# Performance work log

Measured on AMD Instinct MI355X. Metric: run time of the kernel, lower is better.

## Reference

```python
import jax, jax.numpy as jnp
import numpy as np

N = 100000   # num nodes
E = 1000000  # num edges
IN = 64      # in_channels
H = 64       # hidden_dim
RESCUE_SCALE = 0.01


def setup_inputs() -> dict:
    key = jax.random.key(0)
    ks = jax.random.split(key, 8)
    x = jax.random.normal(ks[0], (N, IN), jnp.float32)
    edge_index = jax.random.randint(ks[1], (2, E), 0, N, dtype=jnp.int64)
    edge_weight = jax.random.uniform(ks[2], (E,), jnp.float32)
    glorot = lambda k, sh, fan: jax.random.normal(k, sh, jnp.float32) / np.sqrt(fan).astype(np.float32)
    W1 = glorot(ks[3], (IN, H), IN); b1 = jnp.zeros((H,), jnp.float32)
    W2 = glorot(ks[4], (H, H), H);  b2 = jnp.zeros((H,), jnp.float32)
    Wn = glorot(ks[5], (H, 1), H);  bn = jnp.zeros((1,), jnp.float32)
    Wr = glorot(ks[6], (H, 1), H);  br = jnp.zeros((1,), jnp.float32)
    return {"x": x, "edge_index": edge_index, "edge_weight": edge_weight,
            "W1": W1, "b1": b1, "W2": W2, "b2": b2,
            "Wn": Wn, "bn": bn, "Wr": Wr, "br": br}


def gcn_conv(x, src, dst, ew, W, b):
    # PyG GCNConv: linear first, then symmetric-normalized scatter-add aggregation.
    x = x @ W                                              # [N, H]
    deg = jax.ops.segment_sum(ew, dst, num_segments=N)     # weighted in-degree
    dinv = jnp.where(deg > 0, jax.lax.rsqrt(deg), 0.0)     # deg^{-1/2}, inf -> 0
    norm = dinv[src] * ew * dinv[dst]                      # [E+N]
    out = jax.ops.segment_sum(x[src] * norm[:, None], dst, num_segments=N)
    return out + b


def reference(x, edge_index, edge_weight, W1, b1, W2, b2, Wn, bn, Wr, br):
    # add self-loops with weight 1 (GCNConv default)
    loop = jnp.arange(N, dtype=edge_index.dtype)
    src = jnp.concatenate([edge_index[0], loop])
    dst = jnp.concatenate([edge_index[1], loop])
    ew = jnp.concatenate([edge_weight, jnp.ones((N,), edge_weight.dtype)])

    h = jax.nn.relu(gcn_conv(x, src, dst, ew, W1, b1))
    h = jax.nn.relu(gcn_conv(h, src, dst, ew, W2, b2))

    node_logits = (h @ Wn + bn).squeeze(-1)                # [N]
    node_selector = jax.nn.softmax(node_logits, axis=0)
    rescue_ratios = jax.nn.sigmoid((h @ Wr + br).squeeze(-1)) * RESCUE_SCALE
    return node_selector, rescue_ratios
```

## Files before the change

### kernel.cpp

```cpp
#include <hip/hip_runtime.h>
#include <hip/hip_fp16.h>
#include <math.h>

#define NN 100000
#define NE 1000000
#define CAP 32
#define OVCAP 4096
#define NEB 3907
#define NTILE 6250
#define RB 256

typedef _Float16 half8 __attribute__((ext_vector_type(8)));
typedef float f32x4 __attribute__((ext_vector_type(4)));


__global__ __launch_bounds__(256) void k_bucket(const int* __restrict__ src,
                                                const int* __restrict__ dst,
                                                const float* __restrict__ ew,
                                                int* __restrict__ cnt,
                                                int2* __restrict__ bucket,
                                                int4* __restrict__ ovf,
                                                int* __restrict__ ovf_n) {
  int e = blockIdx.x * 256 + threadIdx.x;
  if (e < NE) {
    int s = src[e];
    int d = dst[e];
    float w = ew[e];
    int pos = atomicAdd(&cnt[d], 1);
    if (pos < CAP) {
      bucket[d * CAP + pos] = make_int2(s, __float_as_int(w));
    } else {
      int t = atomicAdd(ovf_n, 1);
      if (t < OVCAP) ovf[t] = make_int4(s, d, __float_as_int(w), 0);
    }
  }
}


__global__ __launch_bounds__(256) void k_degsum(const int* __restrict__ cnt,
                                                const int2* __restrict__ bucket,
                                                const int4* __restrict__ ovf,
                                                const int* __restrict__ ovf_n,
                                                float* __restrict__ dinv) {
  int i = blockIdx.x * 256 + threadIdx.x;
  if (i >= NN) return;
  int c = cnt[i];
  int cc = c < CAP ? c : CAP;
  float dsum = 1.0f;
  const int2* bk = bucket + (size_t)i * CAP;
  for (int j = 0; j < cc; ++j) dsum += __int_as_float(bk[j].y);
  if (c > CAP) {
    int on = ovf_n[0]; if (on > OVCAP) on = OVCAP;
    for (int t = 0; t < on; ++t) {
      int4 o = ovf[t];
      if (o.y == i) dsum += __int_as_float(o.z);
    }
  }
  dinv[i] = 1.0f / sqrtf(dsum);
}


__device__ __forceinline__ void stage_B_lds(const float* __restrict__ W,
                                            _Float16* __restrict__ ldsB) {
  for (int u = threadIdx.x; u < 512; u += 256) {
    int slane = u & 63, ts = u >> 6;
    int t = ts >> 1, s = ts & 1;
    int qq = slane >> 4, ll = slane & 15;
#pragma unroll
    for (int j = 0; j < 8; ++j)
      ldsB[u * 8 + j] = (_Float16)W[(s * 32 + qq * 8 + j) * 64 + t * 16 + ll];
  }
}

__global__ __launch_bounds__(256) void k_gemm_mfma_f32(const float* __restrict__ X,
                                                       const float* __restrict__ W,
                                                       const float* __restrict__ dinv,
                                                       __half* __restrict__ Y) {
  __shared__ _Float16 ldsB[4096];
  stage_B_lds(W, ldsB);
  __syncthreads();
  int lane = threadIdx.x & 63;
  int l15 = lane & 15, q = lane >> 4;
  half8 bfr[4][2];
#pragma unroll
  for (int t = 0; t < 4; ++t)
#pragma unroll
    for (int s = 0; s < 2; ++s)
      bfr[t][s] = *(half8*)&ldsB[((t * 2 + s) * 64 + lane) * 8];

  int wid = blockIdx.x * 4 + (threadIdx.x >> 6);
  for (int tile = wid; tile < NTILE; tile += 2048) {
    int row = tile * 16 + l15;
    f32x4 acc[4] = {{0.f,0.f,0.f,0.f},{0.f,0.f,0.f,0.f},
                    {0.f,0.f,0.f,0.f},{0.f,0.f,0.f,0.f}};
#pragma unroll
    for (int s = 0; s < 2; ++s) {
      const float* ap = X + (size_t)row * 64 + s * 32 + q * 8;
      float4 a0 = *(const float4*)ap;
      float4 a1 = *(const float4*)(ap + 4);
      half8 af;
      af[0] = (_Float16)a0.x; af[1] = (_Float16)a0.y;
      af[2] = (_Float16)a0.z; af[3] = (_Float16)a0.w;
      af[4] = (_Float16)a1.x; af[5] = (_Float16)a1.y;
      af[6] = (_Float16)a1.z; af[7] = (_Float16)a1.w;
#pragma unroll
      for (int t = 0; t < 4; ++t)
        acc[t] = __builtin_amdgcn_mfma_f32_16x16x32_f16(af, bfr[t][s], acc[t], 0, 0, 0);
    }
#pragma unroll
    for (int r = 0; r < 4; ++r) {
      int rw = tile * 16 + q * 4 + r;
      float dv = dinv[rw];
#pragma unroll
      for (int t = 0; t < 4; ++t)
        Y[(size_t)rw * 64 + t * 16 + l15] = __float2half(acc[t][r] * dv);
    }
  }
}

__global__ __launch_bounds__(256) void k_gemm_mfma_f16(const __half* __restrict__ X,
                                                       const float* __restrict__ W,
                                                       const float* __restrict__ dinv,
                                                       __half* __restrict__ Y) {
  __shared__ _Float16 ldsB[4096];
  stage_B_lds(W, ldsB);
  __syncthreads();
  int lane = threadIdx.x & 63;
  int l15 = lane & 15, q = lane >> 4;
  half8 bfr[4][2];
#pragma unroll
  for (int t = 0; t < 4; ++t)
#pragma unroll
    for (int s = 0; s < 2; ++s)
      bfr[t][s] = *(half8*)&ldsB[((t * 2 + s) * 64 + lane) * 8];

  int wid = blockIdx.x * 4 + (threadIdx.x >> 6);
  for (int tile = wid; tile < NTILE; tile += 2048) {
    int row = tile * 16 + l15;
    f32x4 acc[4] = {{0.f,0.f,0.f,0.f},{0.f,0.f,0.f,0.f},
                    {0.f,0.f,0.f,0.f},{0.f,0.f,0.f,0.f}};
#pragma unroll
    for (int s = 0; s < 2; ++s) {
      half8 af = *(const half8*)((const _Float16*)X + (size_t)row * 64 + s * 32 + q * 8);
#pragma unroll
      for (int t = 0; t < 4; ++t)
        acc[t] = __builtin_amdgcn_mfma_f32_16x16x32_f16(af, bfr[t][s], acc[t], 0, 0, 0);
    }
#pragma unroll
    for (int r = 0; r < 4; ++r) {
      int rw = tile * 16 + q * 4 + r;
      float dv = dinv[rw];
#pragma unroll
      for (int t = 0; t < 4; ++t)
        Y[(size_t)rw * 64 + t * 16 + l15] = __float2half(acc[t][r] * dv);
    }
  }
}


__device__ __forceinline__ float4 h4load(const __half* p) {
  float2 raw = *(const float2*)p;
  __half2 a = *(__half2*)&raw.x;
  __half2 b = *(__half2*)&raw.y;
  float2 fa = __half22float2(a), fb = __half22float2(b);
  return make_float4(fa.x, fa.y, fb.x, fb.y);
}

__device__ __forceinline__ float4 gather_node(const __half* __restrict__ xw,
                                              const int* __restrict__ cnt,
                                              const int2* __restrict__ bucket,
                                              const int4* __restrict__ ovf,
                                              const int* __restrict__ ovf_n,
                                              int node, int l) {
  int c = cnt[node];
  int cc = c < CAP ? c : CAP;
  const int4* bk4 = (const int4*)(bucket + (size_t)node * CAP);
  float4 acc = make_float4(0.f, 0.f, 0.f, 0.f);

  int j = 0;
  for (; j + 4 <= cc; j += 4) {
    int4 pa = bk4[j >> 1];
    int4 pb = bk4[(j >> 1) + 1];
    const float4 x0 = h4load(xw + (size_t)pa.x * 64 + l * 4);
    const float4 x1 = h4load(xw + (size_t)pa.z * 64 + l * 4);
    const float4 x2 = h4load(xw + (size_t)pb.x * 64 + l * 4);
    const float4 x3 = h4load(xw + (size_t)pb.z * 64 + l * 4);
    float v0 = __int_as_float(pa.y);
    float v1 = __int_as_float(pa.w);
    float v2 = __int_as_float(pb.y);
    float v3 = __int_as_float(pb.w);
    acc.x = fmaf(x0.x, v0, acc.x); acc.y = fmaf(x0.y, v0, acc.y);
    acc.z = fmaf(x0.z, v0, acc.z); acc.w = fmaf(x0.w, v0, acc.w);
    acc.x = fmaf(x1.x, v1, acc.x); acc.y = fmaf(x1.y, v1, acc.y);
    acc.z = fmaf(x1.z, v1, acc.z); acc.w = fmaf(x1.w, v1, acc.w);
    acc.x = fmaf(x2.x, v2, acc.x); acc.y = fmaf(x2.y, v2, acc.y);
    acc.z = fmaf(x2.z, v2, acc.z); acc.w = fmaf(x2.w, v2, acc.w);
    acc.x = fmaf(x3.x, v3, acc.x); acc.y = fmaf(x3.y, v3, acc.y);
    acc.z = fmaf(x3.z, v3, acc.z); acc.w = fmaf(x3.w, v3, acc.w);
  }
  const int2* bk = (const int2*)bk4;
  for (; j < cc; ++j) {
    int2 E = bk[j];
    const float4 xa = h4load(xw + (size_t)E.x * 64 + l * 4);
    float v = __int_as_float(E.y);
    acc.x = fmaf(xa.x, v, acc.x); acc.y = fmaf(xa.y, v, acc.y);
    acc.z = fmaf(xa.z, v, acc.z); acc.w = fmaf(xa.w, v, acc.w);
  }
  if (c > CAP) {
    int on = ovf_n[0]; if (on > OVCAP) on = OVCAP;
    for (int t = 0; t < on; ++t) {
      int4 o = ovf[t];
      if (o.y == node) {
        const float4 xa = h4load(xw + (size_t)o.x * 64 + l * 4);
        float v = __int_as_float(o.z);
        acc.x = fmaf(xa.x, v, acc.x); acc.y = fmaf(xa.y, v, acc.y);
        acc.z = fmaf(xa.z, v, acc.z); acc.w = fmaf(xa.w, v, acc.w);
      }
    }
  }
  const float4 xs = h4load(xw + (size_t)node * 64 + l * 4);
  acc.x += xs.x; acc.y += xs.y; acc.z += xs.z; acc.w += xs.w;
  return acc;
}


__global__ __launch_bounds__(256) void k_gather_l1(const __half* __restrict__ xw,
                                                   const float* __restrict__ dinv,
                                                   const int* __restrict__ cnt,
                                                   const int2* __restrict__ bucket,
                                                   const int4* __restrict__ ovf,
                                                   const int* __restrict__ ovf_n,
                                                   const float* __restrict__ b,
                                                   __half* __restrict__ h) {
  int l = threadIdx.x & 15;
  int node = blockIdx.x * 16 + (threadIdx.x >> 4);
  float4 acc = gather_node(xw, cnt, bucket, ovf, ovf_n, node, l);
  float di = dinv[node];
  const float4 b4 = *(const float4*)(b + l * 4);
  __half2 h01 = __float22half2_rn(make_float2(fmaxf(fmaf(acc.x, di, b4.x), 0.f),
                                              fmaxf(fmaf(acc.y, di, b4.y), 0.f)));
  __half2 h23 = __float22half2_rn(make_float2(fmaxf(fmaf(acc.z, di, b4.z), 0.f),
                                              fmaxf(fmaf(acc.w, di, b4.w), 0.f)));
  float2 st;
  st.x = *(float*)&h01;
  st.y = *(float*)&h23;
  *(float2*)(h + (size_t)node * 64 + l * 4) = st;
}


__global__ __launch_bounds__(256) void k_gather_l2_heads(const __half* __restrict__ xw,
                                                         const float* __restrict__ dinv,
                                                         const int* __restrict__ cnt,
                                                         const int2* __restrict__ bucket,
                                                         const int4* __restrict__ ovf,
                                                         const int* __restrict__ ovf_n,
                                                         const float* __restrict__ b2,
                                                         const float* __restrict__ Wn,
                                                         const float* __restrict__ bn,
                                                         const float* __restrict__ Wr,
                                                         const float* __restrict__ br,
                                                         float* __restrict__ logits,
                                                         float* __restrict__ rr,
                                                         float* __restrict__ part) {
  __shared__ float s[256];
  int l = threadIdx.x & 15;
  int node = blockIdx.x * 16 + (threadIdx.x >> 4);
  float4 acc = gather_node(xw, cnt, bucket, ovf, ovf_n, node, l);
  float di = dinv[node];
  const float4 b4 = *(const float4*)(b2 + l * 4);
  float4 r;
  r.x = fmaxf(fmaf(acc.x, di, b4.x), 0.f); r.y = fmaxf(fmaf(acc.y, di, b4.y), 0.f);
  r.z = fmaxf(fmaf(acc.z, di, b4.z), 0.f); r.w = fmaxf(fmaf(acc.w, di, b4.w), 0.f);
  const float4 wn4 = *(const float4*)(Wn + l * 4);
  const float4 wr4 = *(const float4*)(Wr + l * 4);
  float an = r.x * wn4.x + r.y * wn4.y + r.z * wn4.z + r.w * wn4.w;
  float ar = r.x * wr4.x + r.y * wr4.y + r.z * wr4.z + r.w * wr4.w;
#pragma unroll
  for (int m = 8; m > 0; m >>= 1) {
    an += __shfl_xor(an, m, 64);
    ar += __shfl_xor(ar, m, 64);
  }
  float lg = an + bn[0];
  if (l == 0) {
    logits[node] = lg;
    float xr = ar + br[0];
    rr[node] = 0.01f / (1.0f + expf(-xr));
  }
  s[threadIdx.x] = lg;
  __syncthreads();
  for (int w = 128; w > 0; w >>= 1) {
    if (threadIdx.x < w) s[threadIdx.x] = fmaxf(s[threadIdx.x], s[threadIdx.x + w]);
    __syncthreads();
  }
  if (threadIdx.x == 0) part[blockIdx.x] = s[0];
}


__global__ __launch_bounds__(256) void k_smax_final(const float* __restrict__ part,
                                                    float* __restrict__ gmax) {
  __shared__ float s[256];
  float m = -INFINITY;
  for (int i = threadIdx.x; i < NTILE; i += 256) m = fmaxf(m, part[i]);
  s[threadIdx.x] = m;
  __syncthreads();
  for (int w = 128; w > 0; w >>= 1) {
    if (threadIdx.x < w) s[threadIdx.x] = fmaxf(s[threadIdx.x], s[threadIdx.x + w]);
    __syncthreads();
  }
  if (threadIdx.x == 0) gmax[0] = s[0];
}

__global__ __launch_bounds__(256) void k_sexp(const float* __restrict__ logits,
                                              const float* __restrict__ gmax,
                                              float* __restrict__ sel,
                                              float* __restrict__ gsum) {
  __shared__ float s[256];
  float m = gmax[0];
  float acc = 0.0f;
  for (int i = blockIdx.x * 256 + threadIdx.x; i < NN; i += RB * 256) {
    float e = expf(logits[i] - m);
    sel[i] = e;
    acc += e;
  }
  s[threadIdx.x] = acc;
  __syncthreads();
  for (int w = 128; w > 0; w >>= 1) {
    if (threadIdx.x < w) s[threadIdx.x] += s[threadIdx.x + w];
    __syncthreads();
  }
  if (threadIdx.x == 0) unsafeAtomicAdd(gsum, s[0]);
}

__global__ __launch_bounds__(256) void k_snorm(float* __restrict__ sel,
                                               const float* __restrict__ gsum) {
  int i = blockIdx.x * 256 + threadIdx.x;
  if (i < NN) sel[i] *= (1.0f / gsum[0]);
}


extern "C" void kernel_launch(void* const* d_in, const int* in_sizes, int n_in,
                              void* d_out, int out_size, void* d_ws, size_t ws_size,
                              hipStream_t stream) {
  const float* x  = (const float*)d_in[0];
  const int*   ei = (const int*)d_in[1];
  const float* ew = (const float*)d_in[2];
  const float* W1 = (const float*)d_in[3];
  const float* b1 = (const float*)d_in[4];
  const float* W2 = (const float*)d_in[5];
  const float* b2 = (const float*)d_in[6];
  const float* Wn = (const float*)d_in[7];
  const float* bn = (const float*)d_in[8];
  const float* Wr = (const float*)d_in[9];
  const float* br = (const float*)d_in[10];
  const int* src = ei;
  const int* dst = ei + NE;

  char* wsb = (char*)d_ws;
  __half* xw     = (__half*)wsb;
  __half* h      = (__half*)(wsb + 12800000);
  float*  dinv   = (float*)(wsb + 25600000);
  float*  logits = (float*)(wsb + 26000000);
  int2*   bucket = (int2*)(wsb + 26400000);
  int4*   ovf    = (int4*)(wsb + 52000000);
  int*    cnt    = (int*)(wsb + 52065536);
  int*    ovf_n  = cnt + NN;
  float*  gsum   = (float*)(ovf_n + 1);
  float*  gmax   = gsum + 1;
  float*  part1  = gmax + 1;

  float* sel = (float*)d_out;
  float* rr  = (float*)d_out + NN;

  int gN = (NN + 255) / 256;

  hipMemsetAsync(cnt, 0, (size_t)(NN + 2) * 4, stream);

  k_bucket<<<NEB, 256, 0, stream>>>(src, dst, ew, cnt, bucket, ovf, ovf_n);
  k_degsum<<<gN, 256, 0, stream>>>(cnt, bucket, ovf, ovf_n, dinv);

  k_gemm_mfma_f32<<<512, 256, 0, stream>>>(x, W1, dinv, xw);
  k_gather_l1<<<NTILE, 256, 0, stream>>>(xw, dinv, cnt, bucket, ovf, ovf_n, b1, h);

  k_gemm_mfma_f16<<<512, 256, 0, stream>>>(h, W2, dinv, xw);
  k_gather_l2_heads<<<NTILE, 256, 0, stream>>>(xw, dinv, cnt, bucket, ovf, ovf_n,
                                               b2, Wn, bn, Wr, br, logits, rr, part1);

  k_smax_final<<<1, 256, 0, stream>>>(part1, gmax);
  k_sexp<<<RB, 256, 0, stream>>>(logits, gmax, sel, gsum);
  k_snorm<<<gN, 256, 0, stream>>>(sel, gsum);
}
```

Measured before the change: 255.7 us.

## Fuse degree computation into GEMM1, gather-L1 into GEMM2, and softmax max into exp

Degree-normalisation is now computed inside the first GEMM, so the separate degsum kernel is gone. Each warp row computes dinv and shares it by shuffle. The layer-1 gather writes its relu output to LDS and runs the layer-2 MFMA in the same block, which removes the h intermediate round-trip through global memory and a kernel launch. The softmax final max reduction is folded into every k_sexp block, cutting one more launch at the cost of each block re-reading the partial maxima. Per-block W2 staging into LDS for 6250 blocks adds redundant work.

Result: no change. 256.0 us (median of 2 runs) (+0.1%).

```diff
diff --git a/kernel.cpp b/kernel.cpp
--- a/kernel.cpp
+++ b/kernel.cpp
@@ -37,29 +37,6 @@
 }
 
 
-__global__ __launch_bounds__(256) void k_degsum(const int* __restrict__ cnt,
-                                                const int2* __restrict__ bucket,
-                                                const int4* __restrict__ ovf,
-                                                const int* __restrict__ ovf_n,
-                                                float* __restrict__ dinv) {
-  int i = blockIdx.x * 256 + threadIdx.x;
-  if (i >= NN) return;
-  int c = cnt[i];
-  int cc = c < CAP ? c : CAP;
-  float dsum = 1.0f;
-  const int2* bk = bucket + (size_t)i * CAP;
-  for (int j = 0; j < cc; ++j) dsum += __int_as_float(bk[j].y);
-  if (c > CAP) {
-    int on = ovf_n[0]; if (on > OVCAP) on = OVCAP;
-    for (int t = 0; t < on; ++t) {
-      int4 o = ovf[t];
-      if (o.y == i) dsum += __int_as_float(o.z);
-    }
-  }
-  dinv[i] = 1.0f / sqrtf(dsum);
-}
-
-
 __device__ __forceinline__ void stage_B_lds(const float* __restrict__ W,
                                             _Float16* __restrict__ ldsB) {
   for (int u = threadIdx.x; u < 512; u += 256) {
@@ -72,10 +49,36 @@
   }
 }
 
-__global__ __launch_bounds__(256) void k_gemm_mfma_f32(const float* __restrict__ X,
-                                                       const float* __restrict__ W,
-                                                       const float* __restrict__ dinv,
-                                                       __half* __restrict__ Y) {
+
+__device__ __forceinline__ float degsum_row(const int* __restrict__ cnt,
+                                            const int2* __restrict__ bucket,
+                                            const int4* __restrict__ ovf,
+                                            const int* __restrict__ ovf_n,
+                                            int row) {
+  int c = cnt[row];
+  int cc = c < CAP ? c : CAP;
+  float dsum = 1.0f;
+  const int2* bk = bucket + (size_t)row * CAP;
+  for (int j = 0; j < cc; ++j) dsum += __int_as_float(bk[j].y);
+  if (c > CAP) {
+    int on = ovf_n[0]; if (on > OVCAP) on = OVCAP;
+    for (int t = 0; t < on; ++t) {
+      int4 o = ovf[t];
+      if (o.y == row) dsum += __int_as_float(o.z);
+    }
+  }
+  return 1.0f / sqrtf(dsum);
+}
+
+
+__global__ __launch_bounds__(256) void k_gemm1_dinv(const float* __restrict__ X,
+                                                    const float* __restrict__ W,
+                                                    const int* __restrict__ cnt,
+                                                    const int2* __restrict__ bucket,
+                                                    const int4* __restrict__ ovf,
+                                                    const int* __restrict__ ovf_n,
+                                                    float* __restrict__ dinv,
+                                                    __half* __restrict__ Y) {
   __shared__ _Float16 ldsB[4096];
   stage_B_lds(W, ldsB);
   __syncthreads();
@@ -91,6 +94,8 @@
   int wid = blockIdx.x * 4 + (threadIdx.x >> 6);
   for (int tile = wid; tile < NTILE; tile += 2048) {
     int row = tile * 16 + l15;
+    float di = degsum_row(cnt, bucket, ovf, ovf_n, row);
+    if (q == 0) dinv[row] = di;
     f32x4 acc[4] = {{0.f,0.f,0.f,0.f},{0.f,0.f,0.f,0.f},
                     {0.f,0.f,0.f,0.f},{0.f,0.f,0.f,0.f}};
 #pragma unroll
@@ -110,46 +115,7 @@
 #pragma unroll
     for (int r = 0; r < 4; ++r) {
       int rw = tile * 16 + q * 4 + r;
-      float dv = dinv[rw];
-#pragma unroll
-      for (int t = 0; t < 4; ++t)
-        Y[(size_t)rw * 64 + t * 16 + l15] = __float2half(acc[t][r] * dv);
-    }
-  }
-}
-
-__global__ __launch_bounds__(256) void k_gemm_mfma_f16(const __half* __restrict__ X,
-                                                       const float* __restrict__ W,
-                                                       const float* __restrict__ dinv,
-                                                       __half* __restrict__ Y) {
-  __shared__ _Float16 ldsB[4096];
-  stage_B_lds(W, ldsB);
-  __syncthreads();
-  int lane = threadIdx.x & 63;
-  int l15 = lane & 15, q = lane >> 4;
-  half8 bfr[4][2];
-#pragma unroll
-  for (int t = 0; t < 4; ++t)
-#pragma unroll
-    for (int s = 0; s < 2; ++s)
-      bfr[t][s] = *(half8*)&ldsB[((t * 2 + s) * 64 + lane) * 8];
-
-  int wid = blockIdx.x * 4 + (threadIdx.x >> 6);
-  for (int tile = wid; tile < NTILE; tile += 2048) {
-    int row = tile * 16 + l15;
-    f32x4 acc[4] = {{0.f,0.f,0.f,0.f},{0.f,0.f,0.f,0.f},
-                    {0.f,0.f,0.f,0.f},{0.f,0.f,0.f,0.f}};
-#pragma unroll
-    for (int s = 0; s < 2; ++s) {
-      half8 af = *(const half8*)((const _Float16*)X + (size_t)row * 64 + s * 32 + q * 8);
-#pragma unroll
-      for (int t = 0; t < 4; ++t)
-        acc[t] = __builtin_amdgcn_mfma_f32_16x16x32_f16(af, bfr[t][s], acc[t], 0, 0, 0);
-    }
-#pragma unroll
-    for (int r = 0; r < 4; ++r) {
-      int rw = tile * 16 + q * 4 + r;
-      float dv = dinv[rw];
+      float dv = __shfl(di, q * 4 + r, 64);
 #pragma unroll
       for (int t = 0; t < 4; ++t)
         Y[(size_t)rw * 64 + t * 16 + l15] = __float2half(acc[t][r] * dv);
@@ -224,31 +190,54 @@
 }
 
 
-__global__ __launch_bounds__(256) void k_gather_l1(const __half* __restrict__ xw,
-                                                   const float* __restrict__ dinv,
-                                                   const int* __restrict__ cnt,
-                                                   const int2* __restrict__ bucket,
-                                                   const int4* __restrict__ ovf,
-                                                   const int* __restrict__ ovf_n,
-                                                   const float* __restrict__ b,
-                                                   __half* __restrict__ h) {
+__global__ __launch_bounds__(256) void k_gather_gemm2(const __half* __restrict__ xw,
+                                                      const float* __restrict__ dinv,
+                                                      const int* __restrict__ cnt,
+                                                      const int2* __restrict__ bucket,
+                                                      const int4* __restrict__ ovf,
+                                                      const int* __restrict__ ovf_n,
+                                                      const float* __restrict__ b1,
+                                                      const float* __restrict__ W2,
+                                                      __half* __restrict__ Y) {
+  __shared__ _Float16 ldsB[4096];
+  __shared__ _Float16 ldsR[16 * 72];
+  __shared__ float sdi[16];
+  stage_B_lds(W2, ldsB);
+
   int l = threadIdx.x & 15;
-  int node = blockIdx.x * 16 + (threadIdx.x >> 4);
+  int g = threadIdx.x >> 4;
+  int node = blockIdx.x * 16 + g;
   float4 acc = gather_node(xw, cnt, bucket, ovf, ovf_n, node, l);
   float di = dinv[node];
-  const float4 b4 = *(const float4*)(b + l * 4);
-  __half2 h01 = __float22half2_rn(make_float2(fmaxf(fmaf(acc.x, di, b4.x), 0.f),
-                                              fmaxf(fmaf(acc.y, di, b4.y), 0.f)));
-  __half2 h23 = __float22half2_rn(make_float2(fmaxf(fmaf(acc.z, di, b4.z), 0.f),
-                                              fmaxf(fmaf(acc.w, di, b4.w), 0.f)));
-  float2 st;
-  st.x = *(float*)&h01;
-  st.y = *(float*)&h23;
-  *(float2*)(h + (size_t)node * 64 + l * 4) = st;
-}
-
-
-__global__ __launch_bounds__(256) void k_gather_l2_heads(const __half* __restrict__ xw,
+  const float4 b4 = *(const float4*)(b1 + l * 4);
+  _Float16* rp = &ldsR[g * 72 + l * 4];
+  rp[0] = (_Float16)fmaxf(fmaf(acc.x, di, b4.x), 0.f);
+  rp[1] = (_Float16)fmaxf(fmaf(acc.y, di, b4.y), 0.f);
+  rp[2] = (_Float16)fmaxf(fmaf(acc.z, di, b4.z), 0.f);
+  rp[3] = (_Float16)fmaxf(fmaf(acc.w, di, b4.w), 0.f);
+  if (l == 0) sdi[g] = di;
+  __syncthreads();
+
+  int lane = threadIdx.x & 63;
+  int l15 = lane & 15, q = lane >> 4;
+  int t = threadIdx.x >> 6;
+  half8 a0 = *(half8*)&ldsR[l15 * 72 + q * 8];
+  half8 a1 = *(half8*)&ldsR[l15 * 72 + 32 + q * 8];
+  half8 bf0 = *(half8*)&ldsB[((t * 2 + 0) * 64 + lane) * 8];
+  half8 bf1 = *(half8*)&ldsB[((t * 2 + 1) * 64 + lane) * 8];
+  f32x4 acc2 = {0.f, 0.f, 0.f, 0.f};
+  acc2 = __builtin_amdgcn_mfma_f32_16x16x32_f16(a0, bf0, acc2, 0, 0, 0);
+  acc2 = __builtin_amdgcn_mfma_f32_16x16x32_f16(a1, bf1, acc2, 0, 0, 0);
+#pragma unroll
+  for (int r = 0; r < 4; ++r) {
+    int rw = blockIdx.x * 16 + q * 4 + r;
+    float dv = sdi[q * 4 + r];
+    Y[(size_t)rw * 64 + t * 16 + l15] = __float2half(acc2[r] * dv);
+  }
+}
+
+
+__global__ __launch_bounds__(256) void k_gather_l2_heads(const __half* __restrict__ xw2,
                                                          const float* __restrict__ dinv,
                                                          const int* __restrict__ cnt,
                                                          const int2* __restrict__ bucket,
@@ -265,7 +254,7 @@
   __shared__ float s[256];
   int l = threadIdx.x & 15;
   int node = blockIdx.x * 16 + (threadIdx.x >> 4);
-  float4 acc = gather_node(xw, cnt, bucket, ovf, ovf_n, node, l);
+  float4 acc = gather_node(xw2, cnt, bucket, ovf, ovf_n, node, l);
   float di = dinv[node];
   const float4 b4 = *(const float4*)(b2 + l * 4);
   float4 r;
@@ -296,8 +285,10 @@
 }
 
 
-__global__ __launch_bounds__(256) void k_smax_final(const float* __restrict__ part,
-                                                    float* __restrict__ gmax) {
+__global__ __launch_bounds__(256) void k_sexp(const float* __restrict__ logits,
+                                              const float* __restrict__ part,
+                                              float* __restrict__ sel,
+                                              float* __restrict__ gsum) {
   __shared__ float s[256];
   float m = -INFINITY;
   for (int i = threadIdx.x; i < NTILE; i += 256) m = fmaxf(m, part[i]);
@@ -307,18 +298,11 @@
     if (threadIdx.x < w) s[threadIdx.x] = fmaxf(s[threadIdx.x], s[threadIdx.x + w]);
     __syncthreads();
   }
-  if (threadIdx.x == 0) gmax[0] = s[0];
-}
-
-__global__ __launch_bounds__(256) void k_sexp(const float* __restrict__ logits,
-                                              const float* __restrict__ gmax,
-                                              float* __restrict__ sel,
-                                              float* __restrict__ gsum) {
-  __shared__ float s[256];
-  float m = gmax[0];
+  float gm = s[0];
+  __syncthreads();
   float acc = 0.0f;
   for (int i = blockIdx.x * 256 + threadIdx.x; i < NN; i += RB * 256) {
-    float e = expf(logits[i] - m);
+    float e = expf(logits[i] - gm);
     sel[i] = e;
     acc += e;
   }
@@ -357,7 +341,7 @@
 
   char* wsb = (char*)d_ws;
   __half* xw     = (__half*)wsb;
-  __half* h      = (__half*)(wsb + 12800000);
+  __half* xw2    = (__half*)(wsb + 12800000);
   float*  dinv   = (float*)(wsb + 25600000);
   float*  logits = (float*)(wsb + 26000000);
   int2*   bucket = (int2*)(wsb + 26400000);
@@ -365,8 +349,7 @@
   int*    cnt    = (int*)(wsb + 52065536);
   int*    ovf_n  = cnt + NN;
   float*  gsum   = (float*)(ovf_n + 1);
-  float*  gmax   = gsum + 1;
-  float*  part1  = gmax + 1;
+  float*  part1  = gsum + 1;
 
   float* sel = (float*)d_out;
   float* rr  = (float*)d_out + NN;
@@ -376,16 +359,15 @@
   hipMemsetAsync(cnt, 0, (size_t)(NN + 2) * 4, stream);
 
   k_bucket<<<NEB, 256, 0, stream>>>(src, dst, ew, cnt, bucket, ovf, ovf_n);
-  k_degsum<<<gN, 256, 0, stream>>>(cnt, bucket, ovf, ovf_n, dinv);
-
-  k_gemm_mfma_f32<<<512, 256, 0, stream>>>(x, W1, dinv, xw);
-  k_gather_l1<<<NTILE, 256, 0, stream>>>(xw, dinv, cnt, bucket, ovf, ovf_n, b1, h);
-
-  k_gemm_mfma_f16<<<512, 256, 0, stream>>>(h, W2, dinv, xw);
-  k_gather_l2_heads<<<NTILE, 256, 0, stream>>>(xw, dinv, cnt, bucket, ovf, ovf_n,
+
+  k_gemm1_dinv<<<512, 256, 0, stream>>>(x, W1, cnt, bucket, ovf, ovf_n, dinv, xw);
+
+  k_gather_gemm2<<<NTILE, 256, 0, stream>>>(xw, dinv, cnt, bucket, ovf, ovf_n,
+                                            b1, W2, xw2);
+
+  k_gather_l2_heads<<<NTILE, 256, 0, stream>>>(xw2, dinv, cnt, bucket, ovf, ovf_n,
                                                b2, Wn, bn, Wr, br, logits, rr, part1);
 
-  k_smax_final<<<1, 256, 0, stream>>>(part1, gmax);
-  k_sexp<<<RB, 256, 0, stream>>>(logits, gmax, sel, gsum);
+  k_sexp<<<RB, 256, 0, stream>>>(logits, part1, sel, gsum);
   k_snorm<<<gN, 256, 0, stream>>>(sel, gsum);
 }
```
